# Performance work log

Hardware: AMD Instinct MI355X
Metric: run time of the kernel (lower is better)

## Reference

```python
import jax, jax.numpy as jnp
import numpy as np


def setup_inputs() -> dict:
    key = jax.random.key(0)
    k1, k2 = jax.random.split(key)
    query = jax.random.normal(k1, (16, 256, 32, 32), dtype=jnp.float32)
    search_map = jax.random.normal(k2, (16, 256, 64, 64), dtype=jnp.float32)
    return {"query": query, "search_map": search_map}


def reference(query, search_map):
    # query: [bs, c, h, w]; search_map: [bs, c, H, W]
    bs, c, h, w = query.shape
    # pad H and W by h//2, w//2 on each side (matches F.pad(left,right,top,bottom))
    padded = jnp.pad(search_map, ((0, 0), (0, 0), (h // 2, h // 2), (w // 2, w // 2)))

    def corr_one(map_, q_):
        # map_: [c, Hp, Wp], q_: [c, h, w]
        # per-sample cross-correlation: the query acts as a single-output conv kernel
        out = jax.lax.conv_general_dilated(
            map_[None],            # [1, c, Hp, Wp]
            q_[None],              # [1, c, h, w] -> OIHW
            window_strides=(1, 1),
            padding="VALID",
            dimension_numbers=("NCHW", "OIHW", "NCHW"),
        )
        return out[0]              # [1, Hout, Wout]

    # vmap over the batch: each sample uses its own query as the kernel
    return jax.vmap(corr_one)(padded, query)  # [bs, 1, Hout, Wout]
```

## Files before the change

kernel.cpp:

```cpp
#include <hip/hip_runtime.h>
#include <stdint.h>

typedef __bf16 bf16x8 __attribute__((ext_vector_type(8)));
typedef float  f32x4  __attribute__((ext_vector_type(4)));
typedef uint32_t u32x4 __attribute__((ext_vector_type(4)));

__device__ __forceinline__ uint16_t f2bf(float f) {
    uint32_t u = __builtin_bit_cast(uint32_t, f);
    u += 0x7FFFu + ((u >> 16) & 1u);
    return (uint16_t)(u >> 16);
}

__global__ __launch_bounds__(256) void qtrans_kernel(const float* __restrict__ Q,
                                                     uint16_t* __restrict__ Qt) {
    __shared__ float T[8 * 1064];
    const int ch = blockIdx.x, b = blockIdx.y;
    const int tid = threadIdx.x;

    const float* src = Q + ((size_t)(b * 256 + ch * 8)) * 1024;
    #pragma unroll
    for (int it = 0; it < 32; ++it) {
        int r = tid + it * 256;
        int c8 = r >> 10, rem = r & 1023;
        T[c8 * 1064 + (rem >> 5) * 33 + (rem & 31)] = src[(size_t)c8 * 1024 + rem];
    }
    __syncthreads();

    uint32_t* dst = (uint32_t*)Qt;
    #pragma unroll
    for (int it = 0; it < 16; ++it) {
        int o2 = tid + it * 256;
        int t  = (o2 & 3) * 2;
        int il = (o2 >> 2) & 15;
        int j  = (o2 >> 6) & 31;
        int ih = (o2 >> 11) & 1;
        float v0 = T[t * 1064 + (ih * 16 + il) * 33 + j];
        float v1 = T[(t + 1) * 1064 + (ih * 16 + il) * 33 + j];
        uint32_t pk = (uint32_t)f2bf(v0) | ((uint32_t)f2bf(v1) << 16);
        size_t oi = ((((size_t)(b * 2 + ih) * 32 + j) * 32 + ch) * 16 + il) * 4 + (t >> 1);
        dst[oi] = pk;
    }
}

__global__ __launch_bounds__(256, 4) void corr_kernel(const float* __restrict__ S,
                                                      const uint16_t* __restrict__ Qt,
                                                      float* __restrict__ out) {
    __shared__ __align__(16) char smem[40960];
    uint16_t* S_l = (uint16_t*)smem;
    float*    Pw  = (float*)smem;

    const int d = blockIdx.x, b = blockIdx.y;
    const int tid = threadIdx.x, wave = tid >> 6, lane = tid & 63;
    const int l15 = lane & 15, l4 = lane >> 4;

    {
        const u32x4 z = {};
        for (int zi = tid; zi < 512; zi += 256) {
            int ch = zi >> 4, r = zi & 15;
            *(u32x4*)&S_l[ch * 640 + r * 8] = z;
        }
    }
    {
        const int sx = tid & 63, w = tid >> 6;
        const float* sp = S + ((size_t)b * 256) * 4096 + (size_t)d * 64;
        #pragma unroll
        for (int k = 0; k < 8; ++k) {
            int ch = w * 8 + k;
            float v[8];
            #pragma unroll
            for (int cc = 0; cc < 8; ++cc)
                v[cc] = sp[(size_t)(ch * 8 + cc) * 4096 + sx];
            u32x4 pk;
            #pragma unroll
            for (int q = 0; q < 4; ++q)
                pk[q] = (uint32_t)f2bf(v[2 * q]) | ((uint32_t)f2bf(v[2 * q + 1]) << 16);
            *(u32x4*)&S_l[ch * 640 + (sx + 16) * 8] = pk;
        }
    }
    __syncthreads();

    f32x4 acc[5][2] = {};

    #pragma unroll
    for (int jj = 0; jj < 4; ++jj) {
        const int j0a = wave + jj * 4;
        const uint16_t* qa0 = Qt + (((size_t)b * 2 + 0) * 32 + j0a) * 4096 + l4 * 128 + l15 * 8;
        const uint16_t* qa1 = Qt + (((size_t)b * 2 + 1) * 32 + j0a) * 4096 + l4 * 128 + l15 * 8;
        const uint16_t* qb0 = qa0 + 16 * 4096;
        const uint16_t* qb1 = qa1 + 16 * 4096;

        int rowt[5];
        #pragma unroll
        for (int t = 0; t < 5; ++t) {
            int rr = j0a + t * 16 + l15;
            rowt[t] = (rr < 80) ? rr : 0;
        }

        #pragma unroll
        for (int s = 0; s < 8; ++s) {
            bf16x8 Ba0 = *(const bf16x8*)(qa0 + s * 512);
            bf16x8 Ba1 = *(const bf16x8*)(qa1 + s * 512);
            bf16x8 Bb0 = *(const bf16x8*)(qb0 + s * 512);
            bf16x8 Bb1 = *(const bf16x8*)(qb1 + s * 512);
            const int chb = (s * 4 + l4) * 640;
            bf16x8 A[5];
            #pragma unroll
            for (int t = 0; t < 5; ++t)
                A[t] = *(const bf16x8*)&S_l[chb + rowt[t] * 8];
            #pragma unroll
            for (int t = 0; t < 5; ++t) {
                acc[t][0] = __builtin_amdgcn_mfma_f32_16x16x32_bf16(A[t], Ba0, acc[t][0], 0, 0, 0);
                acc[t][1] = __builtin_amdgcn_mfma_f32_16x16x32_bf16(A[t], Ba1, acc[t][1], 0, 0, 0);
            }
            #pragma unroll
            for (int t = 1; t < 5; ++t) {
                acc[t - 1][0] = __builtin_amdgcn_mfma_f32_16x16x32_bf16(A[t], Bb0, acc[t - 1][0], 0, 0, 0);
                acc[t - 1][1] = __builtin_amdgcn_mfma_f32_16x16x32_bf16(A[t], Bb1, acc[t - 1][1], 0, 0, 0);
            }
        }
    }

    __syncthreads();
    {
        float* pw = Pw + wave * 2560;
        #pragma unroll
        for (int m = 0; m < 5; ++m)
            #pragma unroll
            for (int n = 0; n < 2; ++n)
                *(f32x4*)&pw[(n * 16 + l15) * 80 + m * 16 + l4 * 4] = acc[m][n];
    }
    __syncthreads();
    for (int e = tid; e < 65 * 32; e += 256) {
        int x = e % 65, i = e / 65;
        int y = d - i + 16;
        if ((unsigned)y < 65u) {
            float v = Pw[0 * 2560 + i * 80 + x] + Pw[1 * 2560 + i * 80 + x]
                    + Pw[2 * 2560 + i * 80 + x] + Pw[3 * 2560 + i * 80 + x];
            atomicAdd(out + ((size_t)b * 4225 + (size_t)y * 65 + x), v);
        }
    }
}

__global__ __launch_bounds__(256) void naive_kernel(const float* __restrict__ Q,
                                                    const float* __restrict__ S,
                                                    float* __restrict__ out) {
    int gid = blockIdx.x * 256 + threadIdx.x;
    if (gid >= 67600) return;
    int b = gid / 4225, r = gid % 4225, y = r / 65, x = r % 65;
    int jlo = 16 - x; if (jlo < 0) jlo = 0;
    int jhi = 80 - x; if (jhi > 32) jhi = 32;
    float acc = 0.f;
    for (int c = 0; c < 256; ++c) {
        const float* Sb = S + ((size_t)(b * 256 + c)) * 4096;
        const float* Qb = Q + ((size_t)(b * 256 + c)) * 1024;
        for (int i = 0; i < 32; ++i) {
            int dd = y + i - 16;
            if ((unsigned)dd >= 64u) continue;
            const float* Sr = Sb + dd * 64 + (x - 16);
            const float* Qr = Qb + i * 32;
            for (int j = jlo; j < jhi; ++j) acc += Sr[j] * Qr[j];
        }
    }
    out[gid] = acc;
}

extern "C" void kernel_launch(void* const* d_in, const int* in_sizes, int n_in,
                              void* d_out, int out_size, void* d_ws, size_t ws_size,
                              hipStream_t stream) {
    (void)in_sizes; (void)n_in; (void)out_size;
    const float* Q = (const float*)d_in[0];
    const float* S = (const float*)d_in[1];
    float* out = (float*)d_out;

    const size_t QT_BYTES = (size_t)16 * 2 * 32 * 32 * 16 * 8 * 2;

    if (ws_size < QT_BYTES) {
        naive_kernel<<<(67600 + 255) / 256, 256, 0, stream>>>(Q, S, out);
        return;
    }
    uint16_t* Qt = (uint16_t*)d_ws;

    hipMemsetAsync(d_out, 0, (size_t)67600 * sizeof(float), stream);
    qtrans_kernel<<<dim3(32, 16), 256, 0, stream>>>(Q, Qt);
    corr_kernel<<<dim3(64, 16), 256, 0, stream>>>(S, Qt, out);
}
```

Baseline: 136.7 us.

## Pipeline search-map staging and prefetch query fragments across MFMA loop

```diff
diff --git a/kernel.cpp b/kernel.cpp
--- a/kernel.cpp
+++ b/kernel.cpp
@@ -55,69 +55,96 @@
 
     {
         const u32x4 z = {};
-        for (int zi = tid; zi < 512; zi += 256) {
-            int ch = zi >> 4, r = zi & 15;
+        #pragma unroll
+        for (int zi = 0; zi < 2; ++zi) {
+            int e = tid + zi * 256;
+            int ch = e >> 4, r = e & 15;
             *(u32x4*)&S_l[ch * 640 + r * 8] = z;
         }
     }
-    {
-        const int sx = tid & 63, w = tid >> 6;
-        const float* sp = S + ((size_t)b * 256) * 4096 + (size_t)d * 64;
-        #pragma unroll
-        for (int k = 0; k < 8; ++k) {
-            int ch = w * 8 + k;
-            float v[8];
+
+    const int sx = lane;
+    const float* sp = S + ((size_t)b * 256) * 4096 + (size_t)d * 64 + sx;
+
+    #pragma unroll
+    for (int k = 0; k < 4; ++k) {
+        const int ch = k * 4 + wave;
+        float v[8];
+        #pragma unroll
+        for (int cc = 0; cc < 8; ++cc)
+            v[cc] = sp[(size_t)(ch * 8 + cc) * 4096];
+        u32x4 pk;
+        #pragma unroll
+        for (int q = 0; q < 4; ++q)
+            pk[q] = (uint32_t)f2bf(v[2 * q]) | ((uint32_t)f2bf(v[2 * q + 1]) << 16);
+        *(u32x4*)&S_l[ch * 640 + (sx + 16) * 8] = pk;
+    }
+
+    const uint16_t* B0 = Qt + (((size_t)b * 2) * 32 + wave) * 4096 + l4 * 128 + l15 * 8;
+
+    bf16x8 Bc0 = *(const bf16x8*)(B0);
+    bf16x8 Bc1 = *(const bf16x8*)(B0 + 131072);
+    bf16x8 Bc2 = *(const bf16x8*)(B0 + 65536);
+    bf16x8 Bc3 = *(const bf16x8*)(B0 + 196608);
+
+    __syncthreads();
+
+    f32x4 acc[5][2] = {};
+    float vs[8];
+
+    #pragma unroll
+    for (int n = 0; n < 32; ++n) {
+        const int s = n >> 2, jj = n & 3;
+
+        if (n == 16) __syncthreads();
+
+        if (n == 0 || n == 3 || n == 6 || n == 9) {
+            const int ch = 16 + (n / 3) * 4 + wave;
             #pragma unroll
             for (int cc = 0; cc < 8; ++cc)
-                v[cc] = sp[(size_t)(ch * 8 + cc) * 4096 + sx];
+                vs[cc] = sp[(size_t)(ch * 8 + cc) * 4096];
+        }
+        if (n == 2 || n == 5 || n == 8 || n == 11) {
+            const int ch = 16 + ((n - 2) / 3) * 4 + wave;
             u32x4 pk;
             #pragma unroll
             for (int q = 0; q < 4; ++q)
-                pk[q] = (uint32_t)f2bf(v[2 * q]) | ((uint32_t)f2bf(v[2 * q + 1]) << 16);
+                pk[q] = (uint32_t)f2bf(vs[2 * q]) | ((uint32_t)f2bf(vs[2 * q + 1]) << 16);
             *(u32x4*)&S_l[ch * 640 + (sx + 16) * 8] = pk;
         }
-    }
-    __syncthreads();
-
-    f32x4 acc[5][2] = {};
-
-    #pragma unroll
-    for (int jj = 0; jj < 4; ++jj) {
+
+        bf16x8 Bn0, Bn1, Bn2, Bn3;
+        if (n < 31) {
+            const int s2 = (n + 1) >> 2, jj2 = (n + 1) & 3;
+            const uint16_t* p = B0 + jj2 * 16384 + s2 * 512;
+            Bn0 = *(const bf16x8*)(p);
+            Bn1 = *(const bf16x8*)(p + 131072);
+            Bn2 = *(const bf16x8*)(p + 65536);
+            Bn3 = *(const bf16x8*)(p + 196608);
+        }
+
         const int j0a = wave + jj * 4;
-        const uint16_t* qa0 = Qt + (((size_t)b * 2 + 0) * 32 + j0a) * 4096 + l4 * 128 + l15 * 8;
-        const uint16_t* qa1 = Qt + (((size_t)b * 2 + 1) * 32 + j0a) * 4096 + l4 * 128 + l15 * 8;
-        const uint16_t* qb0 = qa0 + 16 * 4096;
-        const uint16_t* qb1 = qa1 + 16 * 4096;
-
-        int rowt[5];
+        const int chb = (s * 4 + l4) * 640;
+        bf16x8 A[5];
         #pragma unroll
         for (int t = 0; t < 5; ++t) {
             int rr = j0a + t * 16 + l15;
-            rowt[t] = (rr < 80) ? rr : 0;
-        }
-
-        #pragma unroll
-        for (int s = 0; s < 8; ++s) {
-            bf16x8 Ba0 = *(const bf16x8*)(qa0 + s * 512);
-            bf16x8 Ba1 = *(const bf16x8*)(qa1 + s * 512);
-            bf16x8 Bb0 = *(const bf16x8*)(qb0 + s * 512);
-            bf16x8 Bb1 = *(const bf16x8*)(qb1 + s * 512);
-            const int chb = (s * 4 + l4) * 640;
-            bf16x8 A[5];
-            #pragma unroll
-            for (int t = 0; t < 5; ++t)
-                A[t] = *(const bf16x8*)&S_l[chb + rowt[t] * 8];
-            #pragma unroll
-            for (int t = 0; t < 5; ++t) {
-                acc[t][0] = __builtin_amdgcn_mfma_f32_16x16x32_bf16(A[t], Ba0, acc[t][0], 0, 0, 0);
-                acc[t][1] = __builtin_amdgcn_mfma_f32_16x16x32_bf16(A[t], Ba1, acc[t][1], 0, 0, 0);
-            }
-            #pragma unroll
-            for (int t = 1; t < 5; ++t) {
-                acc[t - 1][0] = __builtin_amdgcn_mfma_f32_16x16x32_bf16(A[t], Bb0, acc[t - 1][0], 0, 0, 0);
-                acc[t - 1][1] = __builtin_amdgcn_mfma_f32_16x16x32_bf16(A[t], Bb1, acc[t - 1][1], 0, 0, 0);
-            }
-        }
+            rr = (rr < 80) ? rr : 0;
+            A[t] = *(const bf16x8*)&S_l[chb + rr * 8];
+        }
+
+        #pragma unroll
+        for (int t = 0; t < 5; ++t) {
+            acc[t][0] = __builtin_amdgcn_mfma_f32_16x16x32_bf16(A[t], Bc0, acc[t][0], 0, 0, 0);
+            acc[t][1] = __builtin_amdgcn_mfma_f32_16x16x32_bf16(A[t], Bc1, acc[t][1], 0, 0, 0);
+        }
+        #pragma unroll
+        for (int t = 1; t < 5; ++t) {
+            acc[t - 1][0] = __builtin_amdgcn_mfma_f32_16x16x32_bf16(A[t], Bc2, acc[t - 1][0], 0, 0, 0);
+            acc[t - 1][1] = __builtin_amdgcn_mfma_f32_16x16x32_bf16(A[t], Bc3, acc[t - 1][1], 0, 0, 0);
+        }
+
+        if (n < 31) { Bc0 = Bn0; Bc1 = Bn1; Bc2 = Bn2; Bc3 = Bn3; }
     }
 
     __syncthreads();
@@ -126,8 +153,8 @@
         #pragma unroll
         for (int m = 0; m < 5; ++m)
             #pragma unroll
-            for (int n = 0; n < 2; ++n)
-                *(f32x4*)&pw[(n * 16 + l15) * 80 + m * 16 + l4 * 4] = acc[m][n];
+            for (int nn = 0; nn < 2; ++nn)
+                *(f32x4*)&pw[(nn * 16 + l15) * 80 + m * 16 + l4 * 4] = acc[m][nn];
     }
     __syncthreads();
     for (int e = tid; e < 65 * 32; e += 256) {
```

Result: slower. 142.3 us (+4.1%).

## Split channel reduction across two blocks, halve LDS, fuse output zeroing

Applied to the files above, without the earlier changes.

```diff
diff --git a/kernel.cpp b/kernel.cpp
--- a/kernel.cpp
+++ b/kernel.cpp
@@ -12,10 +12,16 @@
 }
 
 __global__ __launch_bounds__(256) void qtrans_kernel(const float* __restrict__ Q,
-                                                     uint16_t* __restrict__ Qt) {
+                                                     uint16_t* __restrict__ Qt,
+                                                     float* __restrict__ out) {
     __shared__ float T[8 * 1064];
     const int ch = blockIdx.x, b = blockIdx.y;
     const int tid = threadIdx.x;
+
+    {
+        int g = (b * 32 + ch) * 256 + tid;
+        if (g < 67600) out[g] = 0.f;
+    }
 
     const float* src = Q + ((size_t)(b * 256 + ch * 8)) * 1024;
     #pragma unroll
@@ -42,34 +48,34 @@
     }
 }
 
-__global__ __launch_bounds__(256, 4) void corr_kernel(const float* __restrict__ S,
+__global__ __launch_bounds__(256, 8) void corr_kernel(const float* __restrict__ S,
                                                       const uint16_t* __restrict__ Qt,
                                                       float* __restrict__ out) {
-    __shared__ __align__(16) char smem[40960];
+    __shared__ __align__(16) char smem[20480];
     uint16_t* S_l = (uint16_t*)smem;
     float*    Pw  = (float*)smem;
 
-    const int d = blockIdx.x, b = blockIdx.y;
+    const int bid = blockIdx.x;
+    const int b = bid & 15, d = (bid >> 4) & 63, z = bid >> 10;
     const int tid = threadIdx.x, wave = tid >> 6, lane = tid & 63;
     const int l15 = lane & 15, l4 = lane >> 4;
 
     {
-        const u32x4 z = {};
-        for (int zi = tid; zi < 512; zi += 256) {
-            int ch = zi >> 4, r = zi & 15;
-            *(u32x4*)&S_l[ch * 640 + r * 8] = z;
-        }
+        const u32x4 zz = {};
+        int ch = tid >> 4, r = tid & 15;
+        *(u32x4*)&S_l[ch * 640 + r * 8] = zz;
     }
     {
-        const int sx = tid & 63, w = tid >> 6;
-        const float* sp = S + ((size_t)b * 256) * 4096 + (size_t)d * 64;
-        #pragma unroll
-        for (int k = 0; k < 8; ++k) {
-            int ch = w * 8 + k;
+        const int sx = lane;
+        const float* sp = S + ((size_t)b * 256 + (size_t)z * 128) * 4096
+                            + (size_t)d * 64 + sx;
+        #pragma unroll
+        for (int k = 0; k < 4; ++k) {
+            const int ch = k * 4 + wave;
             float v[8];
             #pragma unroll
             for (int cc = 0; cc < 8; ++cc)
-                v[cc] = sp[(size_t)(ch * 8 + cc) * 4096 + sx];
+                v[cc] = sp[(size_t)(ch * 8 + cc) * 4096];
             u32x4 pk;
             #pragma unroll
             for (int q = 0; q < 4; ++q)
@@ -84,10 +90,11 @@
     #pragma unroll
     for (int jj = 0; jj < 4; ++jj) {
         const int j0a = wave + jj * 4;
-        const uint16_t* qa0 = Qt + (((size_t)b * 2 + 0) * 32 + j0a) * 4096 + l4 * 128 + l15 * 8;
-        const uint16_t* qa1 = Qt + (((size_t)b * 2 + 1) * 32 + j0a) * 4096 + l4 * 128 + l15 * 8;
-        const uint16_t* qb0 = qa0 + 16 * 4096;
-        const uint16_t* qb1 = qa1 + 16 * 4096;
+        const uint16_t* qa0 = Qt + (((size_t)b * 2 + 0) * 32 + j0a) * 4096
+                                 + z * 2048 + l4 * 128 + l15 * 8;
+        const uint16_t* qa1 = qa0 + 131072;
+        const uint16_t* qb0 = qa0 + 65536;
+        const uint16_t* qb1 = qa0 + 196608;
 
         int rowt[5];
         #pragma unroll
@@ -97,7 +104,7 @@
         }
 
         #pragma unroll
-        for (int s = 0; s < 8; ++s) {
+        for (int s = 0; s < 4; ++s) {
             bf16x8 Ba0 = *(const bf16x8*)(qa0 + s * 512);
             bf16x8 Ba1 = *(const bf16x8*)(qa1 + s * 512);
             bf16x8 Bb0 = *(const bf16x8*)(qb0 + s * 512);
@@ -121,21 +128,33 @@
     }
 
     __syncthreads();
-    {
+    if (wave < 2) {
         float* pw = Pw + wave * 2560;
         #pragma unroll
         for (int m = 0; m < 5; ++m)
             #pragma unroll
             for (int n = 0; n < 2; ++n)
                 *(f32x4*)&pw[(n * 16 + l15) * 80 + m * 16 + l4 * 4] = acc[m][n];
+    }
+    __syncthreads();
+    if (wave >= 2) {
+        float* pw = Pw + (wave - 2) * 2560;
+        #pragma unroll
+        for (int m = 0; m < 5; ++m)
+            #pragma unroll
+            for (int n = 0; n < 2; ++n) {
+                const int o = (n * 16 + l15) * 80 + m * 16 + l4 * 4;
+                f32x4 v = *(f32x4*)&pw[o];
+                v += acc[m][n];
+                *(f32x4*)&pw[o] = v;
+            }
     }
     __syncthreads();
     for (int e = tid; e < 65 * 32; e += 256) {
         int x = e % 65, i = e / 65;
         int y = d - i + 16;
         if ((unsigned)y < 65u) {
-            float v = Pw[0 * 2560 + i * 80 + x] + Pw[1 * 2560 + i * 80 + x]
-                    + Pw[2 * 2560 + i * 80 + x] + Pw[3 * 2560 + i * 80 + x];
+            float v = Pw[i * 80 + x] + Pw[2560 + i * 80 + x];
             atomicAdd(out + ((size_t)b * 4225 + (size_t)y * 65 + x), v);
         }
     }
@@ -180,7 +199,6 @@
     }
     uint16_t* Qt = (uint16_t*)d_ws;
 
-    hipMemsetAsync(d_out, 0, (size_t)67600 * sizeof(float), stream);
-    qtrans_kernel<<<dim3(32, 16), 256, 0, stream>>>(Q, Qt);
-    corr_kernel<<<dim3(64, 16), 256, 0, stream>>>(S, Qt, out);
-}
+    qtrans_kernel<<<dim3(32, 16), 256, 0, stream>>>(Q, Qt, out);
+    corr_kernel<<<2048, 256, 0, stream>>>(S, Qt, out);
+}
```

New measurement: 370.8 us. 2.71x slower.
